# Performance work log

Measured on AMD Instinct MI355X. Metric: run time of the kernel, lower is better.

Reference implementation:

```python
import jax, jax.numpy as jnp
import numpy as np

LABEL_SMOOTHING = 0.1


def setup_inputs() -> dict:
    key = jax.random.key(0)
    k1, k2, k3 = jax.random.split(key, 3)
    B, N, D = 16384, 1000, 1000  # code structurally requires D == n_classes == N
    inputs = jax.random.uniform(k1, (B, D), dtype=jnp.float32)
    labels = jax.random.randint(k2, (B,), 0, N, dtype=jnp.int64)
    code_book = jax.random.uniform(k3, (N, D), dtype=jnp.float32)
    return {"inputs": inputs, "labels": labels, "code_book": code_book}


def reference(inputs, labels, code_book):
    # inputs: [B, D], code_book: [N, D], D == N (n_classes)
    n_classes = inputs.shape[1]
    # soft targets with label smoothing (same as scatter_ + smoothing)
    soft_target = jax.nn.one_hot(labels, n_classes, dtype=inputs.dtype)
    soft_target = soft_target * (1.0 - LABEL_SMOOTHING) + LABEL_SMOOTHING / n_classes
    # Hamming similarity: sum_d [o*c + (1-o)*(1-c)]  ==  o@c.T + (1-o)@(1-c).T
    # (algebraic rewrite of the [B, N, D] broadcast in the original; same math)
    similarity = (jnp.einsum("bd,nd->bn", inputs, code_book)
                  + jnp.einsum("bd,nd->bn", 1.0 - inputs, 1.0 - code_book))
    logp = jax.nn.log_softmax(similarity, axis=1)
    return jnp.mean(jnp.sum(-soft_target * logp, axis=1))
```

## Files before the change

kernel.cpp:

```cpp
#include <hip/hip_runtime.h>

typedef __attribute__((ext_vector_type(8))) short bf16x8;
typedef __attribute__((ext_vector_type(4))) float f32x4;

#define AS1 __attribute__((address_space(1)))
#define AS3 __attribute__((address_space(3)))

__device__ static inline void gl2lds16(const void* g, void* l) {
  __builtin_amdgcn_global_load_lds((const AS1 unsigned int*)g, (AS3 unsigned int*)l, 16, 0, 0);
}

__device__ static inline unsigned short f2bf(float x) {
  unsigned int u = __float_as_uint(x);
  unsigned int r = u + 0x7FFFu + ((u >> 16) & 1u);
  return (unsigned short)(r >> 16);
}

__global__ __launch_bounds__(256) void prep_bl_k(
    const float* __restrict__ cb, const int* __restrict__ labraw,
    unsigned short* __restrict__ b, float* __restrict__ rowsum,
    int* __restrict__ labs, float* __restrict__ lin, float* __restrict__ out) {
  const int bx = blockIdx.x, t = threadIdx.x;
  if (bx < 1024) {
    int n = bx;
    float s = 0.f;
#pragma unroll
    for (int j = 0; j < 4; ++j) {
      int c = t + j * 256;
      float v = 0.f;
      if (n < 1000 && c < 1000) v = cb[(size_t)n * 1000 + c];
      s += v;
      b[((size_t)n << 10) + c] = f2bf(v);
    }
    __shared__ float red[256];
    red[t] = s;
    __syncthreads();
    for (int o = 128; o > 0; o >>= 1) {
      if (t < o) red[t] += red[t + o];
      __syncthreads();
    }
    if (t == 0) rowsum[n] = (n < 1000) ? red[0] : 0.f;
  } else {
    __shared__ int nz;
    if (t == 0) nz = 0;
    __syncthreads();
    if (labraw[2 * t + 1] != 0) atomicAdd(&nz, 1);
    __syncthreads();
    bool is64 = (nz < 32);
    int row = (bx - 1024) * 256 + t;
    labs[row] = is64 ? labraw[2 * row] : labraw[row];
    if (bx == 1024 && t == 0) { lin[0] = 0.f; out[0] = 0.f; }
  }
}

__global__ __launch_bounds__(512, 2) void coding_loss_k(
    const float* __restrict__ In,
    const unsigned short* __restrict__ Bg,
    const float* __restrict__ rowsum,
    const int* __restrict__ labels,
    float* __restrict__ Z,
    float* __restrict__ lin) {
  __shared__ __align__(16) unsigned short lds[32768];

  const int t    = threadIdx.x;
  const int lane = t & 63;
  const int w    = t >> 6;
  const int wr   = w >> 2;
  const int wc   = w & 3;
  const int g16  = lane >> 4;
  const int c16  = lane & 15;
  const int ct   = blockIdx.x & 3;
  const int rt   = blockIdx.x >> 2;
  const int r0   = rt << 8;
  const int c0   = ct << 8;

  const int sg  = (t & 3) ^ ((t >> 3) & 3);
  const int rA0 = t >> 2, rA1 = 128 + (t >> 2);
  const float* pA0 = In + (size_t)(r0 + rA0) * 1000 + sg * 8;
  const float* pA1 = In + (size_t)(r0 + rA1) * 1000 + sg * 8;
  size_t b_src[2]; int bdst[2];
#pragma unroll
  for (int i = 0; i < 2; ++i) {
    int ch = i * 512 + t, row = ch >> 2;
    int sgb = (ch & 3) ^ ((row >> 1) & 3);
    b_src[i] = (size_t)(c0 + row) * 1024 + sgb * 8;
    bdst[i] = ch * 8;
  }
  int a_eoff[8], b_eoff[4];
#pragma unroll
  for (int i = 0; i < 8; ++i) {
    int ar = wr * 128 + i * 16 + c16;
    a_eoff[i] = ar * 32 + ((g16 ^ ((ar >> 1) & 3)) << 3);
  }
#pragma unroll
  for (int i = 0; i < 4; ++i) {
    int br = wc * 64 + i * 16 + c16;
    b_eoff[i] = br * 32 + ((g16 ^ ((br >> 1) & 3)) << 3);
  }

  f32x4 acc[8][4];
#pragma unroll
  for (int mi = 0; mi < 8; ++mi)
#pragma unroll
    for (int ni = 0; ni < 4; ++ni) acc[mi][ni] = (f32x4)(0.f);

#define LOADA(js, G0A, G0B, G1A, G1B)                                          \
  {                                                                            \
    if ((js) < 31 || sg == 0) {                                                \
      const float4* q0 = (const float4*)(pA0 + (js) * 32);                     \
      const float4* q1 = (const float4*)(pA1 + (js) * 32);                     \
      G0A = q0[0]; G0B = q0[1]; G1A = q1[0]; G1B = q1[1];                      \
    } else {                                                                   \
      G0A = G0B = G1A = G1B = make_float4(0.f, 0.f, 0.f, 0.f);                 \
    }                                                                          \
  }

#define CVWRA(p, G0A, G0B, G1A, G1B)                                           \
  {                                                                            \
    union { unsigned short u[8]; uint4 v; } w0, w1;                            \
    w0.u[0] = f2bf(2.f * G0A.x); w0.u[1] = f2bf(2.f * G0A.y);                  \
    w0.u[2] = f2bf(2.f * G0A.z); w0.u[3] = f2bf(2.f * G0A.w);                  \
    w0.u[4] = f2bf(2.f * G0B.x); w0.u[5] = f2bf(2.f * G0B.y);                  \
    w0.u[6] = f2bf(2.f * G0B.z); w0.u[7] = f2bf(2.f * G0B.w);                  \
    w1.u[0] = f2bf(2.f * G1A.x); w1.u[1] = f2bf(2.f * G1A.y);                  \
    w1.u[2] = f2bf(2.f * G1A.z); w1.u[3] = f2bf(2.f * G1A.w);                  \
    w1.u[4] = f2bf(2.f * G1B.x); w1.u[5] = f2bf(2.f * G1B.y);                  \
    w1.u[6] = f2bf(2.f * G1B.z); w1.u[7] = f2bf(2.f * G1B.w);                  \
    *(uint4*)(lds + ((p) << 13) + t * 8) = w0.v;                               \
    *(uint4*)(lds + ((p) << 13) + 4096 + t * 8) = w1.v;                        \
  }

#define COMPUTE(p)                                                             \
  {                                                                            \
    const unsigned short* pa = lds + ((p) << 13);                              \
    const unsigned short* pb = lds + 16384 + ((p) << 13);                      \
    bf16x8 af[4], af2[4], bv[4];                                               \
    _Pragma("unroll") for (int i = 0; i < 4; ++i)                              \
        af[i] = *(const bf16x8*)(pa + a_eoff[i]);                              \
    _Pragma("unroll") for (int i = 0; i < 4; ++i)                              \
        bv[i] = *(const bf16x8*)(pb + b_eoff[i]);                              \
    _Pragma("unroll") for (int i = 0; i < 4; ++i)                              \
        af2[i] = *(const bf16x8*)(pa + a_eoff[i + 4]);                         \
    _Pragma("unroll") for (int mi = 0; mi < 4; ++mi)                           \
      _Pragma("unroll") for (int ni = 0; ni < 4; ++ni)                         \
        acc[mi][ni] =                                                          \
            __builtin_amdgcn_mfma_f32_16x16x32_bf16(af[mi], bv[ni], acc[mi][ni], 0, 0, 0); \
    _Pragma("unroll") for (int mi = 0; mi < 4; ++mi)                           \
      _Pragma("unroll") for (int ni = 0; ni < 4; ++ni)                         \
        acc[mi + 4][ni] =                                                      \
            __builtin_amdgcn_mfma_f32_16x16x32_bf16(af2[mi], bv[ni], acc[mi + 4][ni], 0, 0, 0); \
  }

  {
    float4 g0a, g0b, g1a, g1b;
    LOADA(0, g0a, g0b, g1a, g1b);
    gl2lds16(Bg + b_src[0], lds + 16384 + bdst[0]);
    gl2lds16(Bg + b_src[1], lds + 16384 + bdst[1]);
    CVWRA(0, g0a, g0b, g1a, g1b);
    __syncthreads();
  }

  for (int J = 0; J < 31; ++J) {
    const int jn = J + 1;
    float4 g0a, g0b, g1a, g1b;
    LOADA(jn, g0a, g0b, g1a, g1b);
    gl2lds16(Bg + b_src[0] + jn * 32, lds + 16384 + ((jn & 1) << 13) + bdst[0]);
    gl2lds16(Bg + b_src[1] + jn * 32, lds + 16384 + ((jn & 1) << 13) + bdst[1]);
    COMPUTE(J & 1);
    CVWRA(jn & 1, g0a, g0b, g1a, g1b);
    __syncthreads();
  }
  COMPUTE(1);
  __syncthreads();

  float* zbuf = (float*)lds;
  float* lbuf = zbuf + 1024;
  float rs[4]; int gcol[4];
#pragma unroll
  for (int ni = 0; ni < 4; ++ni) {
    gcol[ni] = c0 + wc * 64 + ni * 16 + c16;
    rs[ni]   = rowsum[gcol[ni]];
  }
  float lacc = 0.f;
#pragma unroll
  for (int mi = 0; mi < 8; ++mi) {
#pragma unroll
    for (int r = 0; r < 4; ++r) {
      int lrow = mi * 16 + g16 * 4 + r;
      int labv = labels[r0 + wr * 128 + lrow];
      float e = 0.f;
#pragma unroll
      for (int ni = 0; ni < 4; ++ni) {
        float S = acc[mi][ni][r] - rs[ni];
        e += __expf(S - 40.f);
        lacc += 1e-4f * S;
        if (gcol[ni] == labv) lacc += 0.9f * S;
      }
      e += __shfl_xor(e, 1, 64);
      e += __shfl_xor(e, 2, 64);
      e += __shfl_xor(e, 4, 64);
      e += __shfl_xor(e, 8, 64);
      if (c16 == 0) zbuf[w * 128 + lrow] = e;
    }
  }
#pragma unroll
  for (int d = 1; d < 64; d <<= 1) lacc += __shfl_xor(lacc, d, 64);
  if (lane == 0) lbuf[w] = lacc;
  __syncthreads();
  if (t < 256) {
    int wrg = t >> 7, l7 = t & 127;
    float z = zbuf[(wrg * 4 + 0) * 128 + l7] + zbuf[(wrg * 4 + 1) * 128 + l7] +
              zbuf[(wrg * 4 + 2) * 128 + l7] + zbuf[(wrg * 4 + 3) * 128 + l7];
    Z[ct * 16384 + r0 + t] = z;
  }
  if (t == 0)
    atomicAdd(lin, lbuf[0] + lbuf[1] + lbuf[2] + lbuf[3] +
                   lbuf[4] + lbuf[5] + lbuf[6] + lbuf[7]);
#undef LOADA
#undef CVWRA
#undef COMPUTE
}

__global__ __launch_bounds__(256) void finalize_k(const float* __restrict__ Z,
                                                  const float* __restrict__ lin,
                                                  float* __restrict__ out) {
  int t = threadIdx.x;
  int row = blockIdx.x * 256 + t;
  float v = 40.f + logf(Z[row] + Z[16384 + row] + Z[2 * 16384 + row] + Z[3 * 16384 + row]);
#pragma unroll
  for (int d = 1; d < 64; d <<= 1) v += __shfl_xor(v, d, 64);
  __shared__ float s[4];
  if ((t & 63) == 0) s[t >> 6] = v;
  __syncthreads();
  if (t == 0) {
    float tot = s[0] + s[1] + s[2] + s[3];
    if (blockIdx.x == 0) tot -= lin[0];
    atomicAdd(out, tot * (1.f / 16384.f));
  }
}

extern "C" void kernel_launch(void* const* d_in, const int* in_sizes, int n_in,
                              void* d_out, int out_size, void* d_ws, size_t ws_size,
                              hipStream_t stream) {
  const float* inputs = (const float*)d_in[0];
  const int* labraw   = (const int*)d_in[1];
  const float* code   = (const float*)d_in[2];

  unsigned short* b_bf = (unsigned short*)d_ws;
  float* rowsum        = (float*)(b_bf + (size_t)1024 * 1024);
  float* Z             = rowsum + 1024;
  float* lin           = Z + 4 * 16384;
  int* labs            = (int*)(lin + 1);

  prep_bl_k<<<1088, 256, 0, stream>>>(code, labraw, b_bf, rowsum, labs, lin,
                                      (float*)d_out);
  coding_loss_k<<<256, 512, 0, stream>>>(inputs, b_bf, rowsum, labs, Z, lin);
  finalize_k<<<64, 256, 0, stream>>>(Z, lin, (float*)d_out);
}
```

Baseline: 166.9 us.

## Prefetch A two stages ahead with explicit waitcnt and remap block order

The A-tile global loads now run two K-steps ahead using two register sets, so each load has a full compute iteration to land before its bf16 conversion. Sched barriers and an explicit s_waitcnt replace __syncthreads, so the barrier waits only for the older loads rather than draining every outstanding memory operation. The block index is also remapped so consecutive blocks spread across row and column tiles, which is meant to improve L2 locality for A and B. In exchange, register pressure rises from the extra float4 set, and the hand-written waitcnt immediates must be exactly right or the kernel reads stale LDS.

```diff
diff --git a/kernel.cpp b/kernel.cpp
--- a/kernel.cpp
+++ b/kernel.cpp
@@ -69,8 +69,10 @@
   const int wc   = w & 3;
   const int g16  = lane >> 4;
   const int c16  = lane & 15;
-  const int ct   = blockIdx.x & 3;
-  const int rt   = blockIdx.x >> 2;
+  const int bid  = blockIdx.x;
+  const int L    = ((bid & 7) << 5) | (bid >> 3);
+  const int ct   = L & 3;
+  const int rt   = L >> 2;
   const int r0   = rt << 8;
   const int c0   = ct << 8;
 
@@ -104,28 +106,28 @@
 #pragma unroll
     for (int ni = 0; ni < 4; ++ni) acc[mi][ni] = (f32x4)(0.f);
 
-#define LOADA(js, G0A, G0B, G1A, G1B)                                          \
+#define LOADA(js, R0, R1, R2, R3)                                              \
   {                                                                            \
     if ((js) < 31 || sg == 0) {                                                \
-      const float4* q0 = (const float4*)(pA0 + (js) * 32);                     \
-      const float4* q1 = (const float4*)(pA1 + (js) * 32);                     \
-      G0A = q0[0]; G0B = q0[1]; G1A = q1[0]; G1B = q1[1];                      \
+      const float4* q0 = (const float4*)(pA0 + (size_t)(js) * 32);             \
+      const float4* q1 = (const float4*)(pA1 + (size_t)(js) * 32);             \
+      R0 = q0[0]; R1 = q0[1]; R2 = q1[0]; R3 = q1[1];                          \
     } else {                                                                   \
-      G0A = G0B = G1A = G1B = make_float4(0.f, 0.f, 0.f, 0.f);                 \
+      R0 = R1 = R2 = R3 = make_float4(0.f, 0.f, 0.f, 0.f);                     \
     }                                                                          \
   }
 
-#define CVWRA(p, G0A, G0B, G1A, G1B)                                           \
+#define CVWRA(p, R0, R1, R2, R3)                                               \
   {                                                                            \
     union { unsigned short u[8]; uint4 v; } w0, w1;                            \
-    w0.u[0] = f2bf(2.f * G0A.x); w0.u[1] = f2bf(2.f * G0A.y);                  \
-    w0.u[2] = f2bf(2.f * G0A.z); w0.u[3] = f2bf(2.f * G0A.w);                  \
-    w0.u[4] = f2bf(2.f * G0B.x); w0.u[5] = f2bf(2.f * G0B.y);                  \
-    w0.u[6] = f2bf(2.f * G0B.z); w0.u[7] = f2bf(2.f * G0B.w);                  \
-    w1.u[0] = f2bf(2.f * G1A.x); w1.u[1] = f2bf(2.f * G1A.y);                  \
-    w1.u[2] = f2bf(2.f * G1A.z); w1.u[3] = f2bf(2.f * G1A.w);                  \
-    w1.u[4] = f2bf(2.f * G1B.x); w1.u[5] = f2bf(2.f * G1B.y);                  \
-    w1.u[6] = f2bf(2.f * G1B.z); w1.u[7] = f2bf(2.f * G1B.w);                  \
+    w0.u[0] = f2bf(2.f * R0.x); w0.u[1] = f2bf(2.f * R0.y);                    \
+    w0.u[2] = f2bf(2.f * R0.z); w0.u[3] = f2bf(2.f * R0.w);                    \
+    w0.u[4] = f2bf(2.f * R1.x); w0.u[5] = f2bf(2.f * R1.y);                    \
+    w0.u[6] = f2bf(2.f * R1.z); w0.u[7] = f2bf(2.f * R1.w);                    \
+    w1.u[0] = f2bf(2.f * R2.x); w1.u[1] = f2bf(2.f * R2.y);                    \
+    w1.u[2] = f2bf(2.f * R2.z); w1.u[3] = f2bf(2.f * R2.w);                    \
+    w1.u[4] = f2bf(2.f * R3.x); w1.u[5] = f2bf(2.f * R3.y);                    \
+    w1.u[6] = f2bf(2.f * R3.z); w1.u[7] = f2bf(2.f * R3.w);                    \
     *(uint4*)(lds + ((p) << 13) + t * 8) = w0.v;                               \
     *(uint4*)(lds + ((p) << 13) + 4096 + t * 8) = w1.v;                        \
   }
@@ -151,25 +153,41 @@
             __builtin_amdgcn_mfma_f32_16x16x32_bf16(af2[mi], bv[ni], acc[mi + 4][ni], 0, 0, 0); \
   }
 
-  {
-    float4 g0a, g0b, g1a, g1b;
-    LOADA(0, g0a, g0b, g1a, g1b);
-    gl2lds16(Bg + b_src[0], lds + 16384 + bdst[0]);
-    gl2lds16(Bg + b_src[1], lds + 16384 + bdst[1]);
-    CVWRA(0, g0a, g0b, g1a, g1b);
-    __syncthreads();
-  }
-
-  for (int J = 0; J < 31; ++J) {
-    const int jn = J + 1;
-    float4 g0a, g0b, g1a, g1b;
-    LOADA(jn, g0a, g0b, g1a, g1b);
-    gl2lds16(Bg + b_src[0] + jn * 32, lds + 16384 + ((jn & 1) << 13) + bdst[0]);
-    gl2lds16(Bg + b_src[1] + jn * 32, lds + 16384 + ((jn & 1) << 13) + bdst[1]);
-    COMPUTE(J & 1);
-    CVWRA(jn & 1, g0a, g0b, g1a, g1b);
-    __syncthreads();
-  }
+#define REGION(J, C0, C1, C2, C3, L0, L1, L2, L3, DOLOAD, WAITIMM)             \
+  {                                                                            \
+    const int jn = (J) + 1;                                                    \
+    gl2lds16(Bg + b_src[0] + jn * 32, lds + 16384 + ((jn & 1) << 13) + bdst[0]); \
+    gl2lds16(Bg + b_src[1] + jn * 32, lds + 16384 + ((jn & 1) << 13) + bdst[1]); \
+    if (DOLOAD) { LOADA((J) + 2, L0, L1, L2, L3); }                            \
+    __builtin_amdgcn_sched_barrier(0);                                         \
+    COMPUTE((J) & 1);                                                          \
+    __builtin_amdgcn_sched_barrier(0);                                         \
+    CVWRA(jn & 1, C0, C1, C2, C3);                                             \
+    __builtin_amdgcn_sched_barrier(0);                                         \
+    __builtin_amdgcn_s_waitcnt(WAITIMM);                                       \
+    __builtin_amdgcn_s_barrier();                                              \
+    __builtin_amdgcn_sched_barrier(0);                                         \
+  }
+
+  float4 g0a, g0b, g1a, g1b;
+  float4 h0a, h0b, h1a, h1b;
+
+  gl2lds16(Bg + b_src[0], lds + 16384 + bdst[0]);
+  gl2lds16(Bg + b_src[1], lds + 16384 + bdst[1]);
+  LOADA(0, g0a, g0b, g1a, g1b);
+  LOADA(1, h0a, h0b, h1a, h1b);
+  CVWRA(0, g0a, g0b, g1a, g1b);
+  __builtin_amdgcn_sched_barrier(0);
+  __builtin_amdgcn_s_waitcnt(0x074);
+  __builtin_amdgcn_s_barrier();
+  __builtin_amdgcn_sched_barrier(0);
+
+  for (int j2 = 0; j2 < 15; ++j2) {
+    const int J = j2 * 2;
+    REGION(J,     h0a, h0b, h1a, h1b, g0a, g0b, g1a, g1b, 1, 0x074);
+    REGION(J + 1, g0a, g0b, g1a, g1b, h0a, h0b, h1a, h1b, 1, 0x074);
+  }
+  REGION(30, h0a, h0b, h1a, h1b, g0a, g0b, g1a, g1b, 0, 0x070);
   COMPUTE(1);
   __syncthreads();
 
@@ -219,6 +237,7 @@
 #undef LOADA
 #undef CVWRA
 #undef COMPUTE
+#undef REGION
 }
 
 __global__ __launch_bounds__(256) void finalize_k(const float* __restrict__ Z,
```

After: 155.3 us. 7.0% less time.

## Shrink GEMM tiles to 256x128 with triple-buffered B and grouped block order

Applied to the files above, without the earlier changes.

The main kernel now uses 256-thread blocks on 256x128 output tiles, which doubles the grid to 512 blocks and gives 8 column partial sums that finalize has to combine. The B operand is triple-buffered through direct global-to-LDS loads, and the barriers use explicit waitcnt so one B load stays in flight across iterations. Block indices are remapped so consecutive blocks share column tiles, which should help cache reuse. The cost is re-reading and re-converting each A row tile twice, since there are now 8 column tiles per row tile instead of 4. It also relies on a hand-set waitcnt encoding being correct.

```diff
diff --git a/kernel.cpp b/kernel.cpp
--- a/kernel.cpp
+++ b/kernel.cpp
@@ -53,38 +53,40 @@
   }
 }
 
-__global__ __launch_bounds__(512, 2) void coding_loss_k(
+__global__ __launch_bounds__(256, 2) void coding_loss_k(
     const float* __restrict__ In,
     const unsigned short* __restrict__ Bg,
     const float* __restrict__ rowsum,
     const int* __restrict__ labels,
     float* __restrict__ Z,
     float* __restrict__ lin) {
-  __shared__ __align__(16) unsigned short lds[32768];
+  __shared__ __align__(16) unsigned short lds[28672];
 
   const int t    = threadIdx.x;
   const int lane = t & 63;
   const int w    = t >> 6;
-  const int wr   = w >> 2;
-  const int wc   = w & 3;
+  const int wr   = w >> 1;
+  const int wc   = w & 1;
   const int g16  = lane >> 4;
   const int c16  = lane & 15;
-  const int ct   = blockIdx.x & 3;
-  const int rt   = blockIdx.x >> 2;
+  const int bid  = blockIdx.x;
+  const int L    = ((bid & 7) << 6) | (bid >> 3);
+  const int ct   = L & 7;
+  const int rt   = L >> 3;
   const int r0   = rt << 8;
-  const int c0   = ct << 8;
-
-  const int sg  = (t & 3) ^ ((t >> 3) & 3);
-  const int rA0 = t >> 2, rA1 = 128 + (t >> 2);
-  const float* pA0 = In + (size_t)(r0 + rA0) * 1000 + sg * 8;
-  const float* pA1 = In + (size_t)(r0 + rA1) * 1000 + sg * 8;
+  const int c0   = ct << 7;
+
+  const int sg = (t & 3) ^ ((t >> 3) & 3);
+  const int rA = t >> 2;
+  const float* pA[4];
+#pragma unroll
+  for (int i = 0; i < 4; ++i)
+    pA[i] = In + (size_t)(r0 + rA + 64 * i) * 1000 + sg * 8;
   size_t b_src[2]; int bdst[2];
 #pragma unroll
   for (int i = 0; i < 2; ++i) {
-    int ch = i * 512 + t, row = ch >> 2;
-    int sgb = (ch & 3) ^ ((row >> 1) & 3);
-    b_src[i] = (size_t)(c0 + row) * 1024 + sgb * 8;
-    bdst[i] = ch * 8;
+    b_src[i] = (size_t)(c0 + rA + 64 * i) * 1024 + sg * 8;
+    bdst[i] = (t + 256 * i) * 8;
   }
   int a_eoff[8], b_eoff[4];
 #pragma unroll
@@ -104,43 +106,42 @@
 #pragma unroll
     for (int ni = 0; ni < 4; ++ni) acc[mi][ni] = (f32x4)(0.f);
 
-#define LOADA(js, G0A, G0B, G1A, G1B)                                          \
+  float4 La[8];
+
+#define LOADA(js)                                                              \
   {                                                                            \
     if ((js) < 31 || sg == 0) {                                                \
-      const float4* q0 = (const float4*)(pA0 + (js) * 32);                     \
-      const float4* q1 = (const float4*)(pA1 + (js) * 32);                     \
-      G0A = q0[0]; G0B = q0[1]; G1A = q1[0]; G1B = q1[1];                      \
+      _Pragma("unroll") for (int i = 0; i < 4; ++i) {                          \
+        const float4* q = (const float4*)(pA[i] + (size_t)(js) * 32);          \
+        La[2 * i] = q[0]; La[2 * i + 1] = q[1];                                \
+      }                                                                        \
     } else {                                                                   \
-      G0A = G0B = G1A = G1B = make_float4(0.f, 0.f, 0.f, 0.f);                 \
+      _Pragma("unroll") for (int i = 0; i < 8; ++i)                            \
+        La[i] = make_float4(0.f, 0.f, 0.f, 0.f);                               \
     }                                                                          \
   }
 
-#define CVWRA(p, G0A, G0B, G1A, G1B)                                           \
+#define CVWRA(dst)                                                             \
   {                                                                            \
-    union { unsigned short u[8]; uint4 v; } w0, w1;                            \
-    w0.u[0] = f2bf(2.f * G0A.x); w0.u[1] = f2bf(2.f * G0A.y);                  \
-    w0.u[2] = f2bf(2.f * G0A.z); w0.u[3] = f2bf(2.f * G0A.w);                  \
-    w0.u[4] = f2bf(2.f * G0B.x); w0.u[5] = f2bf(2.f * G0B.y);                  \
-    w0.u[6] = f2bf(2.f * G0B.z); w0.u[7] = f2bf(2.f * G0B.w);                  \
-    w1.u[0] = f2bf(2.f * G1A.x); w1.u[1] = f2bf(2.f * G1A.y);                  \
-    w1.u[2] = f2bf(2.f * G1A.z); w1.u[3] = f2bf(2.f * G1A.w);                  \
-    w1.u[4] = f2bf(2.f * G1B.x); w1.u[5] = f2bf(2.f * G1B.y);                  \
-    w1.u[6] = f2bf(2.f * G1B.z); w1.u[7] = f2bf(2.f * G1B.w);                  \
-    *(uint4*)(lds + ((p) << 13) + t * 8) = w0.v;                               \
-    *(uint4*)(lds + ((p) << 13) + 4096 + t * 8) = w1.v;                        \
-  }
-
-#define COMPUTE(p)                                                             \
+    _Pragma("unroll") for (int i = 0; i < 4; ++i) {                            \
+      union { unsigned short u[8]; uint4 v; } pk;                              \
+      pk.u[0] = f2bf(2.f * La[2 * i].x); pk.u[1] = f2bf(2.f * La[2 * i].y);    \
+      pk.u[2] = f2bf(2.f * La[2 * i].z); pk.u[3] = f2bf(2.f * La[2 * i].w);    \
+      pk.u[4] = f2bf(2.f * La[2 * i + 1].x); pk.u[5] = f2bf(2.f * La[2 * i + 1].y); \
+      pk.u[6] = f2bf(2.f * La[2 * i + 1].z); pk.u[7] = f2bf(2.f * La[2 * i + 1].w); \
+      *(uint4*)((dst) + t * 8 + i * 2048) = pk.v;                              \
+    }                                                                          \
+  }
+
+#define COMPUTE(pa, pb)                                                        \
   {                                                                            \
-    const unsigned short* pa = lds + ((p) << 13);                              \
-    const unsigned short* pb = lds + 16384 + ((p) << 13);                      \
     bf16x8 af[4], af2[4], bv[4];                                               \
     _Pragma("unroll") for (int i = 0; i < 4; ++i)                              \
-        af[i] = *(const bf16x8*)(pa + a_eoff[i]);                              \
+        af[i] = *(const bf16x8*)((pa) + a_eoff[i]);                            \
     _Pragma("unroll") for (int i = 0; i < 4; ++i)                              \
-        bv[i] = *(const bf16x8*)(pb + b_eoff[i]);                              \
+        bv[i] = *(const bf16x8*)((pb) + b_eoff[i]);                            \
     _Pragma("unroll") for (int i = 0; i < 4; ++i)                              \
-        af2[i] = *(const bf16x8*)(pa + a_eoff[i + 4]);                         \
+        af2[i] = *(const bf16x8*)((pa) + a_eoff[i + 4]);                       \
     _Pragma("unroll") for (int mi = 0; mi < 4; ++mi)                           \
       _Pragma("unroll") for (int ni = 0; ni < 4; ++ni)                         \
         acc[mi][ni] =                                                          \
@@ -151,30 +152,52 @@
             __builtin_amdgcn_mfma_f32_16x16x32_bf16(af2[mi], bv[ni], acc[mi + 4][ni], 0, 0, 0); \
   }
 
+  unsigned short* a_rd = lds;
+  unsigned short* a_wr = lds + 8192;
+  unsigned short* b_rd = lds + 16384;
+  unsigned short* b_nx = lds + 16384 + 4096;
+  unsigned short* b_st = lds + 16384 + 8192;
+
+  LOADA(0);
+  gl2lds16(Bg + b_src[0], b_rd + bdst[0]);
+  gl2lds16(Bg + b_src[1], b_rd + bdst[1]);
+  CVWRA(a_rd);
+  LOADA(1);
+  gl2lds16(Bg + b_src[0] + 32, b_nx + bdst[0]);
+  gl2lds16(Bg + b_src[1] + 32, b_nx + bdst[1]);
+  __builtin_amdgcn_sched_barrier(0);
+  __builtin_amdgcn_s_waitcnt(0x07A);
+  __builtin_amdgcn_s_barrier();
+  __builtin_amdgcn_sched_barrier(0);
+
+  for (int J = 0; J < 30; ++J) {
+    COMPUTE(a_rd, b_rd);
+    CVWRA(a_wr);
+    LOADA(J + 2);
+    gl2lds16(Bg + b_src[0] + (size_t)(J + 2) * 32, b_st + bdst[0]);
+    gl2lds16(Bg + b_src[1] + (size_t)(J + 2) * 32, b_st + bdst[1]);
+    __builtin_amdgcn_sched_barrier(0);
+    __builtin_amdgcn_s_waitcnt(0x07A);
+    __builtin_amdgcn_s_barrier();
+    __builtin_amdgcn_sched_barrier(0);
+    unsigned short* x = a_rd; a_rd = a_wr; a_wr = x;
+    x = b_rd; b_rd = b_nx; b_nx = b_st; b_st = x;
+  }
+  COMPUTE(a_rd, b_rd);
+  CVWRA(a_wr);
+  __builtin_amdgcn_sched_barrier(0);
+  __builtin_amdgcn_s_waitcnt(0x070);
+  __builtin_amdgcn_s_barrier();
+  __builtin_amdgcn_sched_barrier(0);
   {
-    float4 g0a, g0b, g1a, g1b;
-    LOADA(0, g0a, g0b, g1a, g1b);
-    gl2lds16(Bg + b_src[0], lds + 16384 + bdst[0]);
-    gl2lds16(Bg + b_src[1], lds + 16384 + bdst[1]);
-    CVWRA(0, g0a, g0b, g1a, g1b);
-    __syncthreads();
-  }
-
-  for (int J = 0; J < 31; ++J) {
-    const int jn = J + 1;
-    float4 g0a, g0b, g1a, g1b;
-    LOADA(jn, g0a, g0b, g1a, g1b);
-    gl2lds16(Bg + b_src[0] + jn * 32, lds + 16384 + ((jn & 1) << 13) + bdst[0]);
-    gl2lds16(Bg + b_src[1] + jn * 32, lds + 16384 + ((jn & 1) << 13) + bdst[1]);
-    COMPUTE(J & 1);
-    CVWRA(jn & 1, g0a, g0b, g1a, g1b);
-    __syncthreads();
-  }
-  COMPUTE(1);
+    unsigned short* x = a_rd; a_rd = a_wr; a_wr = x;
+    x = b_rd; b_rd = b_nx; b_nx = b_st; b_st = x;
+  }
+  COMPUTE(a_rd, b_rd);
   __syncthreads();
 
   float* zbuf = (float*)lds;
-  float* lbuf = zbuf + 1024;
+  float* lbuf = zbuf + 512;
   float rs[4]; int gcol[4];
 #pragma unroll
   for (int ni = 0; ni < 4; ++ni) {
@@ -207,15 +230,12 @@
   for (int d = 1; d < 64; d <<= 1) lacc += __shfl_xor(lacc, d, 64);
   if (lane == 0) lbuf[w] = lacc;
   __syncthreads();
-  if (t < 256) {
+  {
     int wrg = t >> 7, l7 = t & 127;
-    float z = zbuf[(wrg * 4 + 0) * 128 + l7] + zbuf[(wrg * 4 + 1) * 128 + l7] +
-              zbuf[(wrg * 4 + 2) * 128 + l7] + zbuf[(wrg * 4 + 3) * 128 + l7];
-    Z[ct * 16384 + r0 + t] = z;
-  }
-  if (t == 0)
-    atomicAdd(lin, lbuf[0] + lbuf[1] + lbuf[2] + lbuf[3] +
-                   lbuf[4] + lbuf[5] + lbuf[6] + lbuf[7]);
+    float z = zbuf[(wrg * 2 + 0) * 128 + l7] + zbuf[(wrg * 2 + 1) * 128 + l7];
+    Z[(size_t)ct * 16384 + r0 + t] = z;
+  }
+  if (t == 0) atomicAdd(lin, lbuf[0] + lbuf[1] + lbuf[2] + lbuf[3]);
 #undef LOADA
 #undef CVWRA
 #undef COMPUTE
@@ -226,7 +246,10 @@
                                                   float* __restrict__ out) {
   int t = threadIdx.x;
   int row = blockIdx.x * 256 + t;
-  float v = 40.f + logf(Z[row] + Z[16384 + row] + Z[2 * 16384 + row] + Z[3 * 16384 + row]);
+  float zs = 0.f;
+#pragma unroll
+  for (int q = 0; q < 8; ++q) zs += Z[(size_t)q * 16384 + row];
+  float v = 40.f + logf(zs);
 #pragma unroll
   for (int d = 1; d < 64; d <<= 1) v += __shfl_xor(v, d, 64);
   __shared__ float s[4];
@@ -249,11 +272,11 @@
   unsigned short* b_bf = (unsigned short*)d_ws;
   float* rowsum        = (float*)(b_bf + (size_t)1024 * 1024);
   float* Z             = rowsum + 1024;
-  float* lin           = Z + 4 * 16384;
+  float* lin           = Z + 8 * 16384;
   int* labs            = (int*)(lin + 1);
 
   prep_bl_k<<<1088, 256, 0, stream>>>(code, labraw, b_bf, rowsum, labs, lin,
                                       (float*)d_out);
-  coding_loss_k<<<256, 512, 0, stream>>>(inputs, b_bf, rowsum, labs, Z, lin);
+  coding_loss_k<<<512, 256, 0, stream>>>(inputs, b_bf, rowsum, labs, Z, lin);
   finalize_k<<<64, 256, 0, stream>>>(Z, lin, (float*)d_out);
 }
```

New measurement: 155.7 us. 1.07x faster.
